# Kernel tuning notes

Hardware: AMD Instinct MI355X
Metric: run time of the kernel (lower is better)

The kernel has to match this reference:

```python
import jax, jax.numpy as jnp
import numpy as np

N_NEIGHBORS = 8


def setup_inputs() -> dict:
    key = jax.random.key(0)
    kx, ky = jax.random.split(key)
    X = jax.random.normal(kx, (8192, 512), dtype=jnp.float32)
    Y = jax.random.normal(ky, (65536, 512), dtype=jnp.float32)
    return {"X": X, "Y": Y}


def reference(X, Y):
    x_sq = jnp.sum(X * X, axis=1, keepdims=True)          # [NX, 1]
    y_sq = jnp.sum(Y * Y, axis=1)                          # [NY]
    sim = X @ Y.T                                          # [NX, NY]
    distances = x_sq + y_sq - 2.0 * sim                    # [NX, NY]
    # k smallest distances == k largest of negated distances.
    _, indices = jax.lax.top_k(-distances, N_NEIGHBORS)    # [NX, k]
    return indices
```

## Files before the change

kernel.cpp:

```cpp
#include <hip/hip_runtime.h>
#include <math.h>

#define NX 8192
#define NY 65536
#define DIM 512
#define KNN 8

#define BM 128
#define BN 64
#define COLS_PER_CHUNK 2048
#define TILES (COLS_PER_CHUNK / BM)
#define KSTEPS 4
#define NSEG 8
#define NZ 4
#define LPT 8
#define KEEP 8
#define NCAND (NSEG * NZ * KEEP)
#define RESC 16
#define QS 24.f
#define DBIAS (1 << 19)

typedef int i32x4 __attribute__((ext_vector_type(4)));

#define AS1(p) (const __attribute__((address_space(1))) void*)(p)
#define AS3(p) (__attribute__((address_space(3))) void*)(p)

__device__ __forceinline__ int q24(float x) {
    float r = rintf(x * QS);
    r = fminf(127.f, fmaxf(-127.f, r));
    return (int)r;
}

__device__ __forceinline__ unsigned int umin_(unsigned int a, unsigned int b) { return a < b ? a : b; }

template <int K>
__device__ __forceinline__ void pushk_b(unsigned int x, unsigned int (&l)[K]) {
    unsigned int prev = l[0];
    l[0] = umin_(l[0], x);
#pragma unroll
    for (int i = 1; i < K; ++i) {
        unsigned int cur = l[i];
        unsigned int m;
        asm("v_med3_u32 %0, %1, %2, %3" : "=v"(m) : "v"(x), "v"(prev), "v"(cur));
        l[i] = m;
        prev = cur;
    }
}

template <int K>
__device__ __forceinline__ void pushk(unsigned int k, unsigned int (&lst)[K]) {
    if (k >= lst[K - 1]) return;
    lst[K - 1] = k;
#pragma unroll
    for (int p = K - 1; p > 0; --p) {
        if (lst[p] < lst[p - 1]) {
            unsigned int t = lst[p]; lst[p] = lst[p - 1]; lst[p - 1] = t;
        }
    }
}

template <int K>
__device__ __forceinline__ void push(float d, int gi, float (&bd)[K], int (&bi)[K]) {
    if (d > bd[K - 1] || (d == bd[K - 1] && gi >= bi[K - 1])) return;
    bd[K - 1] = d; bi[K - 1] = gi;
#pragma unroll
    for (int p = K - 1; p > 0; --p) {
        bool sw = (bd[p] < bd[p - 1]) || (bd[p] == bd[p - 1] && bi[p] < bi[p - 1]);
        if (sw) {
            float td = bd[p]; bd[p] = bd[p - 1]; bd[p - 1] = td;
            int   ti = bi[p]; bi[p] = bi[p - 1]; bi[p - 1] = ti;
        }
    }
}

__global__ void cvt_q_x(const float* __restrict__ src, signed char* __restrict__ dst, int n8) {
    int i = blockIdx.x * blockDim.x + threadIdx.x;
    if (i >= n8) return;
    const float4* s = (const float4*)src;
    float4 a0 = s[i * 2], a1 = s[i * 2 + 1];
    int lo = (q24(a0.x) & 255) | ((q24(a0.y) & 255) << 8)
           | ((q24(a0.z) & 255) << 16) | ((q24(a0.w) & 255) << 24);
    int hi = (q24(a1.x) & 255) | ((q24(a1.y) & 255) << 8)
           | ((q24(a1.z) & 255) << 16) | ((q24(a1.w) & 255) << 24);
    int2 v; v.x = lo; v.y = hi;
    *(int2*)(dst + (size_t)i * 8) = v;
}

__global__ void ysq_cvt_q(const float* __restrict__ Y, float* __restrict__ ysq,
                          int* __restrict__ ysqq, signed char* __restrict__ Yq) {
    int row  = (blockIdx.x * blockDim.x + threadIdx.x) >> 6;
    int lane = threadIdx.x & 63;
    if (row >= NY) return;
    const float4* yr = reinterpret_cast<const float4*>(Y + (size_t)row * DIM);
    signed char* dst = Yq + (size_t)row * DIM;
    double s = 0.0;
    int sq = 0;
#pragma unroll
    for (int i = 0; i < 2; ++i) {
        float4 v = yr[lane + 64 * i];
        s += (double)v.x * v.x + (double)v.y * v.y + (double)v.z * v.z + (double)v.w * v.w;
        int q0 = q24(v.x), q1 = q24(v.y), q2 = q24(v.z), q3 = q24(v.w);
        sq += q0 * q0 + q1 * q1 + q2 * q2 + q3 * q3;
        int packed = (q0 & 255) | ((q1 & 255) << 8) | ((q2 & 255) << 16) | ((q3 & 255) << 24);
        *(int*)(dst + i * 256 + lane * 4) = packed;
    }
#pragma unroll
    for (int off = 32; off > 0; off >>= 1) {
        s  += __shfl_xor(s, off, 64);
        sq += __shfl_xor(sq, off, 64);
    }
    if (lane == 0) { ysq[row] = (float)s; ysqq[row] = sq + DBIAS; }
}

__global__ __launch_bounds__(256, 3) void knn_coarse_fast(
        const signed char* __restrict__ Xq, const signed char* __restrict__ Yq,
        const int* __restrict__ ysqq,
        unsigned int* __restrict__ cand_k) {
    __shared__ __align__(16) char smem[49152];
    char* As = smem;
    char* Bs = smem + 32768;

    const int tid  = threadIdx.x;
    const int lane = tid & 63;
    const int w    = tid >> 6;
    const int l15  = lane & 15;
    const int lg   = lane >> 4;
    const int xcd  = blockIdx.x;
    const int s_   = blockIdx.y;
    const int z    = blockIdx.z;
    const int row0  = (xcd * 16 + (s_ & 15)) * BN;
    const int yseg  = s_ >> 4;
    const int ybase = yseg * (NY / NSEG) + z * COLS_PER_CHUNK;
    const int slot  = yseg * NZ + z;
    const int m0 = (w >> 1) * 64;
    const int n0 = (w & 1) * 32;

    const int srow = lane >> 3;
    const int scb  = ((lane & 7) ^ srow) << 4;
    const char* pXbase = (const char*)Xq
        + ((size_t)(row0 + w * 16 + srow) << 9) + scb;

#define STAGE(tt, kcc, buf)                                                      \
    {                                                                            \
        const char* pY_ = (const char*)Yq                                        \
            + ((size_t)(ybase + (tt) * BM + w * 32 + srow) << 9)                 \
            + ((kcc) << 7) + scb;                                                \
        const char* pX_ = pXbase + ((kcc) << 7);                                 \
        char* dA_ = As + ((buf) << 14) + (w << 12);                              \
        char* dB_ = Bs + ((buf) << 13) + (w << 11);                              \
        _Pragma("unroll")                                                        \
        for (int q = 0; q < 4; ++q)                                              \
            __builtin_amdgcn_global_load_lds(AS1(pY_ + ((size_t)(q * 8) << 9)),  \
                                             AS3(dA_ + (q << 10)), 16, 0, 0);    \
        _Pragma("unroll")                                                        \
        for (int q = 0; q < 2; ++q)                                              \
            __builtin_amdgcn_global_load_lds(AS1(pX_ + ((size_t)(q * 8) << 9)),  \
                                             AS3(dB_ + (q << 10)), 16, 0, 0);    \
    }

    unsigned int kb_[2][LPT];
#pragma unroll
    for (int nf = 0; nf < 2; ++nf)
#pragma unroll
        for (int m = 0; m < LPT; ++m) kb_[nf][m] = 0xffffffffu;

    STAGE(0, 0, 0);

    for (int t = 0; t < TILES; ++t) {
        const int ytile0 = ybase + t * BM;

        i32x4 yv0, yv1, yv2, yv3;
        {
            const int* yp = ysqq + ytile0 + m0 + lg * 4;
            asm volatile("global_load_dwordx4 %0, %1, off" : "=v"(yv0) : "v"(yp));
            asm volatile("global_load_dwordx4 %0, %1, off" : "=v"(yv1) : "v"(yp + 16));
            asm volatile("global_load_dwordx4 %0, %1, off" : "=v"(yv2) : "v"(yp + 32));
            asm volatile("global_load_dwordx4 %0, %1, off" : "=v"(yv3) : "v"(yp + 48));
        }

        i32x4 acc[4][2];
#pragma unroll
        for (int i = 0; i < 4; ++i)
#pragma unroll
            for (int j = 0; j < 2; ++j) acc[i][j] = (i32x4){0, 0, 0, 0};

#pragma unroll
        for (int kc = 0; kc < KSTEPS; ++kc) {
            const int buf = kc & 1;
            if (kc == 0) asm volatile("s_waitcnt vmcnt(4)" ::: "memory");
            else         asm volatile("s_waitcnt vmcnt(0)" ::: "memory");
            __builtin_amdgcn_sched_barrier(0);
            __builtin_amdgcn_s_barrier();
            if (kc < KSTEPS - 1) {
                STAGE(t, kc + 1, buf ^ 1);
            } else if (t + 1 < TILES) {
                STAGE(t + 1, 0, buf ^ 1);
            }

            const char* Ab = As + (buf << 14);
            const char* Bb = Bs + (buf << 13);
#pragma unroll
            for (int kk = 0; kk < 2; ++kk) {
                const int kbyte = kk * 64 + lg * 16;
                const int sw = kbyte ^ ((l15 & 7) << 4);
                i32x4 af[4], bf[2];
#pragma unroll
                for (int mf = 0; mf < 4; ++mf)
                    af[mf] = *(const i32x4*)(Ab + ((m0 + mf * 16 + l15) << 7) + sw);
#pragma unroll
                for (int nf = 0; nf < 2; ++nf)
                    bf[nf] = *(const i32x4*)(Bb + ((n0 + nf * 16 + l15) << 7) + sw);
                __builtin_amdgcn_s_setprio(1);
#pragma unroll
                for (int mf = 0; mf < 4; ++mf)
#pragma unroll
                    for (int nf = 0; nf < 2; ++nf)
                        acc[mf][nf] = __builtin_amdgcn_mfma_i32_16x16x64_i8(
                            af[mf], bf[nf], acc[mf][nf], 0, 0, 0);
                __builtin_amdgcn_s_setprio(0);
            }
        }

#pragma unroll
        for (int mf = 0; mf < 4; ++mf) {
            const int gib = ytile0 + m0 + mf * 16 + lg * 4;
            const i32x4 yv = (mf == 0) ? yv0 : (mf == 1) ? yv1 : (mf == 2) ? yv2 : yv3;
            int gi[4];
#pragma unroll
            for (int j = 0; j < 4; ++j) gi[j] = gib + j;
#pragma unroll
            for (int nf = 0; nf < 2; ++nf) {
#pragma unroll
                for (int j = 0; j < 4; ++j) {
                    int dqb;
                    asm("v_mad_i32_i24 %0, %1, -2, %2"
                        : "=v"(dqb) : "v"(acc[mf][nf][j]), "v"(yv[j]));
                    unsigned int key = (((unsigned int)dqb << 10) & 0xFFFF0000u)
                                     | (unsigned int)gi[j];
                    pushk_b<LPT>(key, kb_[nf]);
                }
            }
        }
    }
#undef STAGE

    __syncthreads();
    unsigned int* mbuf = (unsigned int*)smem;
    const int mslot = (w >> 1) * 4 + lg;
#pragma unroll
    for (int nf = 0; nf < 2; ++nf) {
        const int r = n0 + nf * 16 + l15;
#pragma unroll
        for (int e = 0; e < LPT; ++e)
            mbuf[r * 66 + mslot * LPT + e] = kb_[nf][e];
    }
    __syncthreads();
    if (tid < 64) {
        unsigned int mk[KEEP];
#pragma unroll
        for (int m = 0; m < KEEP; ++m) mk[m] = 0xffffffffu;
        for (int s2 = 0; s2 < 8; ++s2)
#pragma unroll
            for (int e = 0; e < LPT; ++e)
                pushk_b<KEEP>(mbuf[tid * 66 + s2 * LPT + e], mk);
        const int row = row0 + tid;
        unsigned int* co = cand_k + (size_t)row * NCAND + slot * KEEP;
#pragma unroll
        for (int m = 0; m < KEEP; ++m) co[m] = mk[m];
    }
}

__global__ __launch_bounds__(256) void knn_rescore(
        const float* __restrict__ X, const float* __restrict__ Y,
        const float* __restrict__ ysq,
        const unsigned int* __restrict__ cand_k,
        int* __restrict__ out) {
    __shared__ unsigned int ck[16][NCAND];
    __shared__ int   rci[16][RESC];
    __shared__ float rd[16][RESC];

    const int tid  = threadIdx.x;
    const int row0 = blockIdx.x * 16;

#pragma unroll
    for (int q = 0; q < 16; ++q) {
        const int idx = q * 256 + tid;
        const int r = idx >> 8, j = idx & 255;
        ck[r][j] = cand_k[(size_t)(row0 + r) * NCAND + j];
    }
    __syncthreads();

    if (tid < 16) {
        unsigned int mk[RESC];
#pragma unroll
        for (int m = 0; m < RESC; ++m) mk[m] = 0xffffffffu;
        for (int j = 0; j < NCAND; ++j) pushk<RESC>(ck[tid][j], mk);
#pragma unroll
        for (int m = 0; m < RESC; ++m) rci[tid][m] = (int)(mk[m] & 0xffffu);
    }
    __syncthreads();

    {
        const int r = tid >> 4, c = tid & 15;
        const int row = row0 + r;
        const int yi = rci[r][c];
        const float* xr = X + (size_t)row * DIM;
        const float* yr = Y + (size_t)yi * DIM;
        double acc64 = 0.0;
        for (int kc = 0; kc < DIM; kc += 64) {
            float acc = 0.f;
#pragma unroll
            for (int k4 = 0; k4 < 16; ++k4) {
                float4 xv = *(const float4*)(xr + kc + k4 * 4);
                float4 yv = *(const float4*)(yr + kc + k4 * 4);
                acc = fmaf(xv.x, yv.x, acc);
                acc = fmaf(xv.y, yv.y, acc);
                acc = fmaf(xv.z, yv.z, acc);
                acc = fmaf(xv.w, yv.w, acc);
            }
            acc64 += (double)acc;
        }
        rd[r][c] = (float)((double)ysq[yi] - 2.0 * acc64);
    }
    __syncthreads();

    if (tid < 16) {
        float fd[KNN]; int fi[KNN];
#pragma unroll
        for (int m = 0; m < KNN; ++m) { fd[m] = INFINITY; fi[m] = 0x7fffffff; }
        for (int j = 0; j < RESC; ++j) push<KNN>(rd[tid][j], rci[tid][j], fd, fi);
        const int row = row0 + tid;
#pragma unroll
        for (int m = 0; m < KNN; ++m) out[row * KNN + m] = fi[m];
    }
}

extern "C" void kernel_launch(void* const* d_in, const int* in_sizes, int n_in,
                              void* d_out, int out_size, void* d_ws, size_t ws_size,
                              hipStream_t stream) {
    const float* X = (const float*)d_in[0];
    const float* Y = (const float*)d_in[1];
    int* out = (int*)d_out;

    char* ws = (char*)d_ws;
    float* ysq           = (float*)ws;
    int*   ysqq          = (int*)(ws + 262144);
    unsigned int* cand_k = (unsigned int*)(ws + 524288);
    signed char* Xq      = (signed char*)(ws + 524288 + (size_t)NX * NCAND * 4);
    signed char* Yq      = Xq + (size_t)NX * DIM;

    ysq_cvt_q<<<NY / 4, 256, 0, stream>>>(Y, ysq, ysqq, Yq);
    cvt_q_x<<<(NX * DIM / 8) / 256, 256, 0, stream>>>(X, Xq, NX * DIM / 8);

    dim3 g1(8, 128, NZ);
    knn_coarse_fast<<<g1, 256, 0, stream>>>(Xq, Yq, ysqq, cand_k);

    knn_rescore<<<NX / 16, 256, 0, stream>>>(X, Y, ysq, cand_k, out);
}
```

Baseline: 517.0 us.

## Keep X fragments in registers, prefilter top-3 per tile, stage X rows in LDS

The coarse int8 kernel now loads each wave's X (query) fragments for the full K dimension into registers once, instead of staging X through LDS every k-step. This shrinks LDS to 32KB and removes the B-operand LDS reads and copies. The epilogue keeps a running top-3 per column with med3/min across the 16 values of a tile and pushes only those 3 into the sorted top-8 list, replacing 16 insertions. The rescore kernel caches the 16 X rows in shared memory. Costs are higher VGPR pressure from 64 extra registers, which may hurt occupancy at launch bounds of 3, and candidates are lost if more than 3 of a column's true top-8 fall within one tile.

```diff
diff --git a/kernel.cpp b/kernel.cpp
--- a/kernel.cpp
+++ b/kernel.cpp
@@ -116,9 +116,8 @@
         const signed char* __restrict__ Xq, const signed char* __restrict__ Yq,
         const int* __restrict__ ysqq,
         unsigned int* __restrict__ cand_k) {
-    __shared__ __align__(16) char smem[49152];
+    __shared__ __align__(16) char smem[32768];
     char* As = smem;
-    char* Bs = smem + 32768;
 
     const int tid  = threadIdx.x;
     const int lane = tid & 63;
@@ -135,27 +134,31 @@
     const int m0 = (w >> 1) * 64;
     const int n0 = (w & 1) * 32;
 
+    i32x4 xf[2][4][2];
+    {
+        const char* xb = (const char*)Xq + ((size_t)(row0 + n0 + l15) << 9) + lg * 16;
+#pragma unroll
+        for (int nf = 0; nf < 2; ++nf)
+#pragma unroll
+            for (int kc = 0; kc < 4; ++kc)
+#pragma unroll
+                for (int kk = 0; kk < 2; ++kk)
+                    xf[nf][kc][kk] = *(const i32x4*)(xb + (nf << 13) + kc * 128 + kk * 64);
+    }
+
     const int srow = lane >> 3;
     const int scb  = ((lane & 7) ^ srow) << 4;
-    const char* pXbase = (const char*)Xq
-        + ((size_t)(row0 + w * 16 + srow) << 9) + scb;
 
 #define STAGE(tt, kcc, buf)                                                      \
     {                                                                            \
         const char* pY_ = (const char*)Yq                                        \
             + ((size_t)(ybase + (tt) * BM + w * 32 + srow) << 9)                 \
             + ((kcc) << 7) + scb;                                                \
-        const char* pX_ = pXbase + ((kcc) << 7);                                 \
         char* dA_ = As + ((buf) << 14) + (w << 12);                              \
-        char* dB_ = Bs + ((buf) << 13) + (w << 11);                              \
         _Pragma("unroll")                                                        \
         for (int q = 0; q < 4; ++q)                                              \
             __builtin_amdgcn_global_load_lds(AS1(pY_ + ((size_t)(q * 8) << 9)),  \
                                              AS3(dA_ + (q << 10)), 16, 0, 0);    \
-        _Pragma("unroll")                                                        \
-        for (int q = 0; q < 2; ++q)                                              \
-            __builtin_amdgcn_global_load_lds(AS1(pX_ + ((size_t)(q * 8) << 9)),  \
-                                             AS3(dB_ + (q << 10)), 16, 0, 0);    \
     }
 
     unsigned int kb_[2][LPT];
@@ -198,48 +201,49 @@
             }
 
             const char* Ab = As + (buf << 14);
-            const char* Bb = Bs + (buf << 13);
 #pragma unroll
             for (int kk = 0; kk < 2; ++kk) {
                 const int kbyte = kk * 64 + lg * 16;
                 const int sw = kbyte ^ ((l15 & 7) << 4);
-                i32x4 af[4], bf[2];
+                i32x4 af[4];
 #pragma unroll
                 for (int mf = 0; mf < 4; ++mf)
                     af[mf] = *(const i32x4*)(Ab + ((m0 + mf * 16 + l15) << 7) + sw);
-#pragma unroll
-                for (int nf = 0; nf < 2; ++nf)
-                    bf[nf] = *(const i32x4*)(Bb + ((n0 + nf * 16 + l15) << 7) + sw);
                 __builtin_amdgcn_s_setprio(1);
 #pragma unroll
                 for (int mf = 0; mf < 4; ++mf)
 #pragma unroll
                     for (int nf = 0; nf < 2; ++nf)
                         acc[mf][nf] = __builtin_amdgcn_mfma_i32_16x16x64_i8(
-                            af[mf], bf[nf], acc[mf][nf], 0, 0, 0);
+                            af[mf], xf[nf][kc][kk], acc[mf][nf], 0, 0, 0);
                 __builtin_amdgcn_s_setprio(0);
             }
         }
 
 #pragma unroll
-        for (int mf = 0; mf < 4; ++mf) {
-            const int gib = ytile0 + m0 + mf * 16 + lg * 4;
-            const i32x4 yv = (mf == 0) ? yv0 : (mf == 1) ? yv1 : (mf == 2) ? yv2 : yv3;
-            int gi[4];
-#pragma unroll
-            for (int j = 0; j < 4; ++j) gi[j] = gib + j;
-#pragma unroll
-            for (int nf = 0; nf < 2; ++nf) {
+        for (int nf = 0; nf < 2; ++nf) {
+            unsigned int t0 = 0xffffffffu, t1 = 0xffffffffu, t2 = 0xffffffffu;
+#pragma unroll
+            for (int mf = 0; mf < 4; ++mf) {
+                const i32x4 yv = (mf == 0) ? yv0 : (mf == 1) ? yv1 : (mf == 2) ? yv2 : yv3;
+                const int gib = ytile0 + m0 + mf * 16 + lg * 4;
 #pragma unroll
                 for (int j = 0; j < 4; ++j) {
                     int dqb;
                     asm("v_mad_i32_i24 %0, %1, -2, %2"
                         : "=v"(dqb) : "v"(acc[mf][nf][j]), "v"(yv[j]));
                     unsigned int key = (((unsigned int)dqb << 10) & 0xFFFF0000u)
-                                     | (unsigned int)gi[j];
-                    pushk_b<LPT>(key, kb_[nf]);
+                                     | (unsigned int)(gib + j);
+                    unsigned int n1, n2;
+                    asm("v_med3_u32 %0, %1, %2, %3" : "=v"(n1) : "v"(key), "v"(t0), "v"(t1));
+                    asm("v_med3_u32 %0, %1, %2, %3" : "=v"(n2) : "v"(key), "v"(t1), "v"(t2));
+                    t0 = umin_(t0, key);
+                    t1 = n1; t2 = n2;
                 }
             }
+            pushk_b<LPT>(t0, kb_[nf]);
+            pushk_b<LPT>(t1, kb_[nf]);
+            pushk_b<LPT>(t2, kb_[nf]);
         }
     }
 #undef STAGE
@@ -278,10 +282,17 @@
     __shared__ unsigned int ck[16][NCAND];
     __shared__ int   rci[16][RESC];
     __shared__ float rd[16][RESC];
+    __shared__ __align__(16) float xs[16][516];
 
     const int tid  = threadIdx.x;
     const int row0 = blockIdx.x * 16;
 
+#pragma unroll
+    for (int q = 0; q < 8; ++q) {
+        const int fidx = q * 256 + tid;
+        const int r = fidx >> 7, c4 = fidx & 127;
+        *(float4*)&xs[r][c4 * 4] = *(const float4*)(X + (size_t)(row0 + r) * DIM + c4 * 4);
+    }
 #pragma unroll
     for (int q = 0; q < 16; ++q) {
         const int idx = q * 256 + tid;
@@ -302,9 +313,8 @@
 
     {
         const int r = tid >> 4, c = tid & 15;
-        const int row = row0 + r;
         const int yi = rci[r][c];
-        const float* xr = X + (size_t)row * DIM;
+        const float* xr = xs[r];
         const float* yr = Y + (size_t)yi * DIM;
         double acc64 = 0.0;
         for (int kc = 0; kc < DIM; kc += 64) {
```

Measured after the change: 460.7 us. -10.9%, faster.
